# Kernel optimization log

Hardware: AMD Instinct MI355X
Metric: run time of the kernel (lower is better)

The kernel has to match this reference:

```python
import jax, jax.numpy as jnp
import numpy as np

B, V, L, H = 4, 1024, 2048, 2048
TEMP = 1.0
EPS = 1e-12


def _l2norm(x):
    # F.normalize(x, dim=-1): x / max(||x||, eps)
    n = jnp.linalg.norm(x, axis=-1, keepdims=True)
    return x / jnp.maximum(n, EPS)


def setup_inputs() -> dict:
    key = jax.random.key(0)
    k1, k2, k3, k4 = jax.random.split(key, 4)
    std = H ** (-0.5)
    return {
        "vision_features": jax.random.normal(k1, (B, V, H), dtype=jnp.float32),
        "language_features": jax.random.normal(k2, (B, L, H), dtype=jnp.float32),
        "W_vl": jax.random.normal(k3, (H, 2 * H), dtype=jnp.float32) * std,  # vision_language_gate.weight
        "W_lv": jax.random.normal(k4, (H, 2 * H), dtype=jnp.float32) * std,  # language_vision_gate.weight
    }


def reference(vision_features, language_features, W_vl, W_lv):
    b, vsl, h = vision_features.shape
    lsl = language_features.shape[1]
    max_len = max(vsl, lsl)

    # zero-pad both modalities to max_len along seq dim
    vis_p = jnp.pad(vision_features, ((0, 0), (0, max_len - vsl), (0, 0)))
    lang_p = jnp.pad(language_features, ((0, 0), (0, max_len - lsl), (0, 0)))

    # cosine-similarity attention (fp32 softmax)
    scores = jnp.einsum("bvh,blh->bvl", _l2norm(vis_p), _l2norm(lang_p)) / TEMP
    weights = jax.nn.softmax(scores.astype(jnp.float32), axis=-1).astype(vision_features.dtype)
    fused = jnp.einsum("bvl,blh->bvh", weights, lang_p)  # [b, max_len, h]

    # mean pooling over padded sequences (includes zero padding, as in torch)
    vis_avg = jnp.mean(vis_p, axis=1, keepdims=True)    # [b,1,h]
    lang_avg = jnp.mean(lang_p, axis=1, keepdims=True)  # [b,1,h]

    # sigmoid gates: cat([avg.expand, other], -1) @ W.T
    v2l = jnp.concatenate([jnp.broadcast_to(vis_avg, lang_p.shape), lang_p], axis=-1)
    vl_gate = jax.nn.sigmoid(jnp.einsum("bld,hd->blh", v2l, W_vl))
    l2v = jnp.concatenate([jnp.broadcast_to(lang_avg, vis_p.shape), vis_p], axis=-1)
    lv_gate = jax.nn.sigmoid(jnp.einsum("bvd,hd->bvh", l2v, W_lv))

    vision_output = vision_features + fused[:, :vsl, :] * lv_gate[:, :vsl, :]
    language_output = language_features + fused[:, :lsl, :] * vl_gate[:, :lsl, :]
    return fused[:, :max_len, :], vision_output, language_output
```

## Files before the change

### kernel.cpp

```cpp
#include <hip/hip_runtime.h>

#define H_ 2048

typedef __attribute__((ext_vector_type(8))) short short8;
typedef __attribute__((ext_vector_type(4))) float f32x4;
typedef __attribute__((ext_vector_type(4))) unsigned int u32x4;
typedef __attribute__((ext_vector_type(4))) unsigned short u16x4;

__device__ __forceinline__ unsigned short f2bf(float f) {
  unsigned int u = __builtin_bit_cast(unsigned int, f);
  u += 0x7FFFu + ((u >> 16) & 1u);
  return (unsigned short)(u >> 16);
}
__device__ __forceinline__ float bf2f(unsigned short h) {
  unsigned int u = ((unsigned int)h) << 16;
  return __builtin_bit_cast(float, u);
}
__device__ __forceinline__ unsigned int pk2(float a, float b) {
  return (unsigned int)f2bf(a) | ((unsigned int)f2bf(b) << 16);
}

#define GLDS16(gp, lp)                                                 \
  __builtin_amdgcn_global_load_lds(                                    \
      (const __attribute__((address_space(1))) void*)(gp),             \
      (__attribute__((address_space(3))) void*)(lp), 16, 0, 0)

__global__ __launch_bounds__(256) void prep_rows(
    const float* __restrict__ in, long sIn,
    unsigned short* __restrict__ outBf, long sOut,
    float* __restrict__ rnorm, int validRows) {
  const int tid = threadIdx.x;
  const int r = blockIdx.x, b = blockIdx.y;
  unsigned short* orow = outBf + (long)b * sOut + (long)r * H_ + tid * 8;
  if (r >= validRows) {
    *(u32x4*)orow = (u32x4){0u, 0u, 0u, 0u};
    if (tid == 0) rnorm[b * H_ + r] = 0.f;
    return;
  }
  const float* row = in + (long)b * sIn + (long)r * H_ + tid * 8;
  f32x4 x0 = *(const f32x4*)row;
  f32x4 x1 = *(const f32x4*)(row + 4);
  float ss = x0[0]*x0[0] + x0[1]*x0[1] + x0[2]*x0[2] + x0[3]*x0[3]
           + x1[0]*x1[0] + x1[1]*x1[1] + x1[2]*x1[2] + x1[3]*x1[3];
#pragma unroll
  for (int o = 32; o; o >>= 1) ss += __shfl_xor(ss, o, 64);
  __shared__ float red[4];
  if ((tid & 63) == 0) red[tid >> 6] = ss;
  __syncthreads();
  if (tid == 0) {
    float tot = red[0] + red[1] + red[2] + red[3];
    rnorm[b * H_ + r] = 1.f / fmaxf(sqrtf(tot), 1e-12f);
  }
  u32x4 o;
  o[0] = pk2(x0[0], x0[1]); o[1] = pk2(x0[2], x0[3]);
  o[2] = pk2(x1[0], x1[1]); o[3] = pk2(x1[2], x1[3]);
  *(u32x4*)orow = o;
}

__global__ __launch_bounds__(256) void col_sum_part_bf(
    const unsigned short* __restrict__ visBf,
    const unsigned short* __restrict__ langBf, float* __restrict__ part) {
  const int h = blockIdx.x * 256 + threadIdx.x;
  const int y = blockIdx.y;
  const int which = blockIdx.z & 1;
  const int b = blockIdx.z >> 1;
  const long sP = 2048L * 2048;
  float s = 0.f;
  if (!(which == 0 && y >= 4)) {
    const unsigned short* p =
        (which ? langBf : visBf) + (long)b * sP + (long)(y * 256) * H_ + h;
#pragma unroll 4
    for (int i = 0; i < 256; ++i) s += bf2f(p[(long)i * H_]);
  }
  part[(((long)which * 4 + b) * 8 + y) * H_ + h] = s;
}

__global__ __launch_bounds__(256) void col_sum_final(
    const float* __restrict__ part, float* __restrict__ vavg,
    float* __restrict__ lavg) {
  const int h = blockIdx.x * 256 + threadIdx.x;
  const int b = blockIdx.y;
  const int which = blockIdx.z;
  const float* p = part + (((long)which * 4 + b) * 8) * H_ + h;
  float s = 0.f;
#pragma unroll
  for (int y = 0; y < 8; ++y) s += p[y * H_];
  (which ? lavg : vavg)[b * H_ + h] = s * (1.f / 2048.f);
}

__global__ __launch_bounds__(256) void bias_gemv(
    const float* __restrict__ W, const float* __restrict__ avg,
    float* __restrict__ bias) {
  const int lane = threadIdx.x & 63;
  const int wv = threadIdx.x >> 6;
  const int h = blockIdx.x * 4 + wv;
  const float* wrow = W + (long)h * 4096;
  float a0 = 0.f, a1 = 0.f, a2 = 0.f, a3 = 0.f;
#pragma unroll
  for (int i = 0; i < 8; ++i) {
    const int d = i * 256 + lane * 4;
    f32x4 w4 = *(const f32x4*)(wrow + d);
    f32x4 v0 = *(const f32x4*)(avg + 0 * H_ + d);
    f32x4 v1 = *(const f32x4*)(avg + 1 * H_ + d);
    f32x4 v2 = *(const f32x4*)(avg + 2 * H_ + d);
    f32x4 v3 = *(const f32x4*)(avg + 3 * H_ + d);
    a0 += w4[0]*v0[0] + w4[1]*v0[1] + w4[2]*v0[2] + w4[3]*v0[3];
    a1 += w4[0]*v1[0] + w4[1]*v1[1] + w4[2]*v1[2] + w4[3]*v1[3];
    a2 += w4[0]*v2[0] + w4[1]*v2[1] + w4[2]*v2[2] + w4[3]*v2[3];
    a3 += w4[0]*v3[0] + w4[1]*v3[1] + w4[2]*v3[2] + w4[3]*v3[3];
  }
#pragma unroll
  for (int o = 32; o; o >>= 1) {
    a0 += __shfl_xor(a0, o, 64);
    a1 += __shfl_xor(a1, o, 64);
    a2 += __shfl_xor(a2, o, 64);
    a3 += __shfl_xor(a3, o, 64);
  }
  if (lane == 0) {
    bias[0 * H_ + h] = a0; bias[1 * H_ + h] = a1;
    bias[2 * H_ + h] = a2; bias[3 * H_ + h] = a3;
  }
}

__global__ __launch_bounds__(256) void transpose_bf(
    const unsigned short* __restrict__ in, unsigned short* __restrict__ out) {
  __shared__ unsigned short tle[64][72];
  const int b = blockIdx.z;
  const int l0 = blockIdx.y * 64, h0 = blockIdx.x * 64;
  const unsigned short* inb = in + (long)b * (2048L * 2048);
  unsigned short* outb = out + (long)b * (2048L * 2048);
#pragma unroll
  for (int i = 0; i < 16; ++i) {
    const int idx = i * 256 + threadIdx.x;
    const int r = idx >> 6, c = idx & 63;
    tle[r][c] = inb[(long)(l0 + r) * H_ + h0 + c];
  }
  __syncthreads();
#pragma unroll
  for (int i = 0; i < 16; ++i) {
    const int idx = i * 256 + threadIdx.x;
    const int r = idx >> 6, c = idx & 63;
    outb[(long)(h0 + r) * H_ + l0 + c] = tle[c][r];
  }
}

__global__ __launch_bounds__(256) void extract_whi(
    const float* __restrict__ Wvl, const float* __restrict__ Wlv,
    unsigned short* __restrict__ WvlHi, unsigned short* __restrict__ WlvHi) {
  const int h = blockIdx.x;
  const int which = blockIdx.y;
  const float* src = (which ? Wlv : Wvl) + (long)h * 4096 + 2048 + threadIdx.x * 8;
  unsigned short* dst = (which ? WlvHi : WvlHi) + (long)h * H_ + threadIdx.x * 8;
  f32x4 x0 = *(const f32x4*)src;
  f32x4 x1 = *(const f32x4*)(src + 4);
  u32x4 o;
  o[0] = pk2(x0[0], x0[1]); o[1] = pk2(x0[2], x0[3]);
  o[2] = pk2(x1[0], x1[1]); o[3] = pk2(x1[2], x1[3]);
  *(u32x4*)dst = o;
}

__global__ __launch_bounds__(256) void bcast_fused(
    const float* __restrict__ lavg, float* __restrict__ fused) {
  const int b = blockIdx.y;
  const long r = 1024 + blockIdx.x;
  const int c = threadIdx.x * 8;
  f32x4 v0 = *(const f32x4*)(lavg + b * H_ + c);
  f32x4 v1 = *(const f32x4*)(lavg + b * H_ + c + 4);
  float* dst = fused + (long)b * (2048L * 2048) + r * H_ + c;
  *(f32x4*)dst = v0;
  *(f32x4*)(dst + 4) = v1;
}

__global__ __launch_bounds__(256) void softmax_rows(unsigned short* __restrict__ S) {
  const int tid = threadIdx.x;
  const int lane = tid & 63, wv = tid >> 6;
  const int b = blockIdx.x >> 10;
  const int r = blockIdx.x & 1023;
  unsigned short* rowp =
      S + (long)b * (2048L * 2048) + (long)r * H_ + tid * 8;
  u32x4 raw = *(const u32x4*)rowp;
  float v[8];
#pragma unroll
  for (int i = 0; i < 4; ++i) {
    v[2 * i]     = bf2f((unsigned short)(raw[i] & 0xFFFFu));
    v[2 * i + 1] = bf2f((unsigned short)(raw[i] >> 16));
  }
  float mx = v[0];
#pragma unroll
  for (int i = 1; i < 8; ++i) mx = fmaxf(mx, v[i]);
#pragma unroll
  for (int o = 32; o; o >>= 1) mx = fmaxf(mx, __shfl_xor(mx, o, 64));
  __shared__ float red[4];
  if (lane == 0) red[wv] = mx;
  __syncthreads();
  const float MX = fmaxf(fmaxf(red[0], red[1]), fmaxf(red[2], red[3]));
  float p[8], s = 0.f;
#pragma unroll
  for (int i = 0; i < 8; ++i) { p[i] = __expf(v[i] - MX); s += p[i]; }
#pragma unroll
  for (int o = 32; o; o >>= 1) s += __shfl_xor(s, o, 64);
  __syncthreads();
  if (lane == 0) red[wv] = s;
  __syncthreads();
  const float inv = 1.f / (red[0] + red[1] + red[2] + red[3]);
  u32x4 o;
#pragma unroll
  for (int i = 0; i < 4; ++i) o[i] = pk2(p[2 * i] * inv, p[2 * i + 1] * inv);
  *(u32x4*)rowp = o;
}

struct EpArgs {
  unsigned short* Sout; const float* rv; const float* rl;
  float* Fout;
  const unsigned short* residBf; const float* fusedIn;
  const float* bias; float* Oout;
  long sResid, sFused, sOut;
  const unsigned short* A2; const unsigned short* B2;
  const unsigned short* residBf2; const float* bias2; float* Oout2;
  long sResid2, sOut2;
  const float* lavg;
};

#define BAR_ asm volatile("s_barrier" ::: "memory")
#define WAITV_(n) asm volatile("s_waitcnt vmcnt(" #n ")" ::: "memory")
#define LGKM0_ asm volatile("s_waitcnt lgkmcnt(0)" ::: "memory")
#define SB_ __builtin_amdgcn_sched_barrier(0)

template <int MODE>
__global__ __launch_bounds__(256, 2) void gemm_nt(
    const unsigned short* __restrict__ A, long sA,
    const unsigned short* __restrict__ B, long sB, EpArgs ep) {
  __shared__ unsigned short LDS[32768];

  const int tid = threadIdx.x;
  const int lane = tid & 63;
  const int wave = tid >> 6;

  const int gx = gridDim.x, gy = gridDim.y;
  const int nwg = gx * gy * gridDim.z;
  const int lin = blockIdx.x + gx * (blockIdx.y + gy * blockIdx.z);
  const int swz = (lin & 7) * (nwg >> 3) + (lin >> 3);
  const int bx = swz % gx;
  const int rest = swz / gx;
  const int by = rest % gy;
  const int b = rest / gy;
  const int bn = bx << 7;

  int bm;
  bool second = false;
  const unsigned short* Ab;
  const unsigned short* Bb;
  const unsigned short* RbBf = nullptr;
  const float *Fb = nullptr, *biasb = nullptr;
  float* Ob = nullptr;
  if (MODE == 3) {
    second = (by >= 16);
    bm = (second ? by - 16 : by) << 7;
    Ab = (second ? ep.A2 : A) + (long)b * sA;
    Bb = second ? ep.B2 : B;
    RbBf = (second ? ep.residBf2 : ep.residBf) +
           (long)b * (second ? ep.sResid2 : ep.sResid);
    Ob = (second ? ep.Oout2 : ep.Oout) +
         (long)b * (second ? ep.sOut2 : ep.sOut);
    biasb = (second ? ep.bias2 : ep.bias) + b * H_;
    Fb = ep.fusedIn + (long)b * ep.sFused;
  } else {
    bm = by << 7;
    Ab = A + (long)b * sA;
    Bb = B + (long)b * sB;
  }

  const int srow = tid >> 3;
  const int colOff = (((tid & 7) ^ (srow & 7)) << 3);
  const unsigned short* gA = Ab + (long)(bm + srow) * H_ + colOff;
  const unsigned short* gB = Bb + (long)(bn + srow) * H_ + colOff;
  const int ldst = wave * 512;

#define STAGE_(kt, P)                                               \
  do {                                                              \
    const unsigned short* a_ = gA + (kt) * 64;                      \
    const unsigned short* b_ = gB + (kt) * 64;                      \
    GLDS16(a_,           &LDS[(P) * 16384 + 0     + ldst]);         \
    GLDS16(a_ + 32 * H_, &LDS[(P) * 16384 + 2048  + ldst]);         \
    GLDS16(a_ + 64 * H_, &LDS[(P) * 16384 + 4096  + ldst]);         \
    GLDS16(a_ + 96 * H_, &LDS[(P) * 16384 + 6144  + ldst]);         \
    GLDS16(b_,           &LDS[(P) * 16384 + 8192  + ldst]);         \
    GLDS16(b_ + 32 * H_, &LDS[(P) * 16384 + 10240 + ldst]);         \
    GLDS16(b_ + 64 * H_, &LDS[(P) * 16384 + 12288 + ldst]);         \
    GLDS16(b_ + 96 * H_, &LDS[(P) * 16384 + 14336 + ldst]);         \
  } while (0)

  const int row16 = lane & 15;
  const int kg = lane >> 4;
  const int wr = (wave >> 1) << 6;
  const int wc = (wave & 1) << 6;
  const int x0 = ((kg ^ (row16 & 7)) << 4);
  const int x1 = (((4 + kg) ^ (row16 & 7)) << 4);

  const unsigned bAk0 = (unsigned)(unsigned long long)(
      __attribute__((address_space(3))) const void*)LDS +
      (unsigned)((wr + row16) * 128 + x0);
  const unsigned bAk1 = bAk0 + (unsigned)(x1 - x0);
  const unsigned bBk0 = (unsigned)(unsigned long long)(
      __attribute__((address_space(3))) const void*)LDS +
      (unsigned)(16384 + (wc + row16) * 128 + x0);
  const unsigned bBk1 = bBk0 + (unsigned)(x1 - x0);

#define DSRD_(dst, base, off) \
  asm volatile("ds_read_b128 %0, %1 offset:" #off : "=v"(dst) : "v"(base))

  f32x4 acc[4][4];
#pragma unroll
  for (int m = 0; m < 4; ++m)
#pragma unroll
    for (int n = 0; n < 4; ++n) acc[m][n] = (f32x4){0.f, 0.f, 0.f, 0.f};
  short8 aF[4][2], bF[4][2];

#define RDALL_P0                                           \
  do {                                                     \
    DSRD_(aF[0][0], bAk0, 0);    DSRD_(aF[1][0], bAk0, 2048);  \
    DSRD_(aF[2][0], bAk0, 4096); DSRD_(aF[3][0], bAk0, 6144);  \
    DSRD_(aF[0][1], bAk1, 0);    DSRD_(aF[1][1], bAk1, 2048);  \
    DSRD_(aF[2][1], bAk1, 4096); DSRD_(aF[3][1], bAk1, 6144);  \
    DSRD_(bF[0][0], bBk0, 0);    DSRD_(bF[1][0], bBk0, 2048);  \
    DSRD_(bF[2][0], bBk0, 4096); DSRD_(bF[3][0], bBk0, 6144);  \
    DSRD_(bF[0][1], bBk1, 0);    DSRD_(bF[1][1], bBk1, 2048);  \
    DSRD_(bF[2][1], bBk1, 4096); DSRD_(bF[3][1], bBk1, 6144);  \
  } while (0)
#define RDALL_P1                                                   \
  do {                                                             \
    DSRD_(aF[0][0], bAk0, 32768); DSRD_(aF[1][0], bAk0, 34816);   \
    DSRD_(aF[2][0], bAk0, 36864); DSRD_(aF[3][0], bAk0, 38912);   \
    DSRD_(aF[0][1], bAk1, 32768); DSRD_(aF[1][1], bAk1, 34816);   \
    DSRD_(aF[2][1], bAk1, 36864); DSRD_(aF[3][1], bAk1, 38912);   \
    DSRD_(bF[0][0], bBk0, 32768); DSRD_(bF[1][0], bBk0, 34816);   \
    DSRD_(bF[2][0], bBk0, 36864); DSRD_(bF[3][0], bBk0, 38912);   \
    DSRD_(bF[0][1], bBk1, 32768); DSRD_(bF[1][1], bBk1, 34816);   \
    DSRD_(bF[2][1], bBk1, 36864); DSRD_(bF[3][1], bBk1, 38912);   \
  } while (0)

#define MFMA32_                                                             \
  do {                                                                      \
    __builtin_amdgcn_s_setprio(1);                                          \
    _Pragma("unroll") for (int ks_ = 0; ks_ < 2; ++ks_)                     \
    _Pragma("unroll") for (int m_ = 0; m_ < 4; ++m_)                        \
    _Pragma("unroll") for (int n_ = 0; n_ < 4; ++n_)                        \
        acc[m_][n_] = __builtin_amdgcn_mfma_f32_16x16x32_bf16(              \
            aF[m_][ks_], bF[n_][ks_], acc[m_][n_], 0, 0, 0);                \
    __builtin_amdgcn_s_setprio(0);                                          \
  } while (0)

  STAGE_(0, 0); STAGE_(1, 1);
  WAITV_(8);
  BAR_;

  for (int tt = 0; tt < 15; ++tt) {
    const int t2 = tt * 2;
    RDALL_P0; LGKM0_; SB_;
    BAR_;
    STAGE_(t2 + 2, 0);
    WAITV_(8);
    BAR_;
    MFMA32_;
    RDALL_P1; LGKM0_; SB_;
    BAR_;
    STAGE_(t2 + 3, 1);
    WAITV_(8);
    BAR_;
    MFMA32_;
  }
  RDALL_P0; LGKM0_; SB_;
  BAR_;
  WAITV_(0);
  BAR_;
  MFMA32_;
  RDALL_P1; LGKM0_; SB_;
  MFMA32_;

  const int cr0 = bm + wr + kg * 4;
  const int cc0 = bn + wc + row16;

  if (MODE == 0) {
    float rvv[4][4], rlv[4];
#pragma unroll
    for (int m = 0; m < 4; ++m)
#pragma unroll
      for (int j = 0; j < 4; ++j) rvv[m][j] = ep.rv[b * H_ + cr0 + m * 16 + j];
#pragma unroll
    for (int n = 0; n < 4; ++n) rlv[n] = ep.rl[b * H_ + cc0 + n * 16];
    unsigned short* Sb = ep.Sout + (long)b * (H_ * (long)H_);
#pragma unroll
    for (int m = 0; m < 4; ++m)
#pragma unroll
      for (int n = 0; n < 4; ++n)
#pragma unroll
        for (int j = 0; j < 4; ++j) {
          const long idx = (long)(cr0 + m * 16 + j) * H_ + cc0 + n * 16;
          Sb[idx] = f2bf(acc[m][n][j] * rvv[m][j] * rlv[n]);
        }
  } else {
    float* LF = (float*)LDS;
    __syncthreads();
    const int lwr = wr + kg * 4;
    const int lwc = wc + row16;
#pragma unroll
    for (int m = 0; m < 4; ++m)
#pragma unroll
      for (int n = 0; n < 4; ++n)
#pragma unroll
        for (int j = 0; j < 4; ++j) {
          const int r = lwr + m * 16 + j;
          const int c = lwc + n * 16;
          LF[r * 128 + ((c + 4 * r) & 127)] = acc[m][n][j];
        }
    __syncthreads();
    const int r8 = tid >> 5;
    const int c4 = (tid & 31) * 4;
    if (MODE == 1) {
      float* Fo = ep.Fout + (long)b * (H_ * (long)H_);
#pragma unroll
      for (int it = 0; it < 16; ++it) {
        const int r = it * 8 + r8;
        f32x4 v = *(const f32x4*)&LF[r * 128 + ((c4 + 4 * r) & 127)];
        *(f32x4*)&Fo[(long)(bm + r) * H_ + bn + c4] = v;
      }
    } else {
      const f32x4 bvv = *(const f32x4*)&biasb[bn + c4];
      const bool useLavg = (!second) && (bm >= 1024);
      f32x4 lavgv = (f32x4){0.f, 0.f, 0.f, 0.f};
      if (useLavg) lavgv = *(const f32x4*)&ep.lavg[b * H_ + bn + c4];
#pragma unroll
      for (int it = 0; it < 16; ++it) {
        const int r = it * 8 + r8;
        f32x4 v = *(const f32x4*)&LF[r * 128 + ((c4 + 4 * r) & 127)];
        const long off = (long)(bm + r) * H_ + bn + c4;
        const f32x4 fv = useLavg ? lavgv : *(const f32x4*)&Fb[off];
        const u16x4 rb4 = *(const u16x4*)&RbBf[off];
        f32x4 o;
#pragma unroll
        for (int k = 0; k < 4; ++k) {
          const float x = v[k] + bvv[k];
          const float g = 1.f / (1.f + __expf(-x));
          o[k] = bf2f(rb4[k]) + fv[k] * g;
        }
        *(f32x4*)&Ob[off] = o;
      }
    }
  }
#undef STAGE_
#undef DSRD_
#undef RDALL_P0
#undef RDALL_P1
#undef MFMA32_
}

extern "C" void kernel_launch(void* const* d_in, const int* in_sizes, int n_in,
                              void* d_out, int out_size, void* d_ws,
                              size_t ws_size, hipStream_t stream) {
  (void)in_sizes; (void)n_in; (void)out_size; (void)ws_size;
  const float* vis = (const float*)d_in[0];
  const float* lang = (const float*)d_in[1];
  const float* Wvl = (const float*)d_in[2];
  const float* Wlv = (const float*)d_in[3];

  float* out = (float*)d_out;
  float* fused = out;
  float* vis_out = out + 16777216;
  float* lang_out = out + 25165824;
  unsigned short* S = (unsigned short*)lang_out;
  unsigned short* langT = (unsigned short*)vis_out;

  char* w = (char*)d_ws;
  unsigned short* vis_bf = (unsigned short*)w;
  unsigned short* lang_bf = (unsigned short*)(w + 33554432);
  unsigned short* WvlHi = (unsigned short*)(w + 67108864);
  unsigned short* WlvHi = (unsigned short*)(w + 75497472);
  float* rv      = (float*)(w + 83886080);
  float* rl      = (float*)(w + 83918848);
  float* vavg    = (float*)(w + 83951616);
  float* lavg    = (float*)(w + 83984384);
  float* bias_vl = (float*)(w + 84017152);
  float* bias_lv = (float*)(w + 84049920);
  float* part    = (float*)(w + 84082688);

  const long sV = 1024L * 2048, sL = 2048L * 2048, sP = 2048L * 2048;

  prep_rows<<<dim3(2048, 4), 256, 0, stream>>>(vis, sV, vis_bf, sP, rv, 1024);
  prep_rows<<<dim3(2048, 4), 256, 0, stream>>>(lang, sL, lang_bf, sP, rl, 2048);
  col_sum_part_bf<<<dim3(8, 8, 8), 256, 0, stream>>>(vis_bf, lang_bf, part);
  col_sum_final<<<dim3(8, 4, 2), 256, 0, stream>>>(part, vavg, lavg);
  bias_gemv<<<512, 256, 0, stream>>>(Wvl, vavg, bias_vl);
  bias_gemv<<<512, 256, 0, stream>>>(Wlv, lavg, bias_lv);
  transpose_bf<<<dim3(32, 32, 4), 256, 0, stream>>>(lang_bf, langT);
  extract_whi<<<dim3(2048, 2), 256, 0, stream>>>(Wvl, Wlv, WvlHi, WlvHi);
  bcast_fused<<<dim3(1024, 4), 256, 0, stream>>>(lavg, fused);

  EpArgs e1 = {};
  e1.Sout = S; e1.rv = rv; e1.rl = rl;
  gemm_nt<0><<<dim3(16, 8, 4), 256, 0, stream>>>(vis_bf, sP, lang_bf, sP, e1);

  softmax_rows<<<4096, 256, 0, stream>>>(S);

  EpArgs e2 = {};
  e2.Fout = fused;
  gemm_nt<1><<<dim3(16, 8, 4), 256, 0, stream>>>(S, sP, langT, sP, e2);

  EpArgs e34 = {};
  e34.residBf = lang_bf; e34.sResid = sP;
  e34.fusedIn = fused; e34.sFused = sP;
  e34.bias = bias_vl; e34.Oout = lang_out; e34.sOut = sL;
  e34.A2 = vis_bf; e34.B2 = WlvHi;
  e34.residBf2 = vis_bf; e34.sResid2 = sP;
  e34.bias2 = bias_lv; e34.Oout2 = vis_out; e34.sOut2 = sV;
  e34.lavg = lavg;
  gemm_nt<3><<<dim3(16, 24, 4), 256, 0, stream>>>(lang_bf, sP, WvlHi, 0L, e34);
}
```

Measured before the change: 290.5 us.

## Switch GEMM to 32x32x16 MFMA and stage all epilogues through LDS

Each wave's 64x64 GEMM tile now uses a 2x2 grid of 32x32x16 bf16 MFMAs instead of a 4x4 grid of 16x16x32 ones. LDS fragment addressing is re-derived for the new layout. This is meant to raise arithmetic intensity per LDS read and cut MFMA issue count. The score-GEMM epilogue now goes through the same swizzled LDS staging as the other modes, so the bf16 S writes become coalesced 4-wide stores instead of scattered 2-byte stores. The vision prep_rows launch is halved so the padded rows are no longer written; this assumes the workspace already holds zeros there, which is a correctness risk if the workspace is not cleared.

Result: slower. 310.8 us (+7.0%).

```diff
diff --git a/kernel.cpp b/kernel.cpp
--- a/kernel.cpp
+++ b/kernel.cpp
@@ -4,6 +4,7 @@
 
 typedef __attribute__((ext_vector_type(8))) short short8;
 typedef __attribute__((ext_vector_type(4))) float f32x4;
+typedef __attribute__((ext_vector_type(16))) float f32x16;
 typedef __attribute__((ext_vector_type(4))) unsigned int u32x4;
 typedef __attribute__((ext_vector_type(4))) unsigned short u16x4;
 
@@ -290,62 +291,67 @@
     GLDS16(b_ + 96 * H_, &LDS[(P) * 16384 + 14336 + ldst]);         \
   } while (0)
 
-  const int row16 = lane & 15;
-  const int kg = lane >> 4;
+  const int row32 = lane & 31;
+  const int khalf = lane >> 5;
+  const int r7 = row32 & 7;
   const int wr = (wave >> 1) << 6;
   const int wc = (wave & 1) << 6;
-  const int x0 = ((kg ^ (row16 & 7)) << 4);
-  const int x1 = (((4 + kg) ^ (row16 & 7)) << 4);
-
-  const unsigned bAk0 = (unsigned)(unsigned long long)(
-      __attribute__((address_space(3))) const void*)LDS +
-      (unsigned)((wr + row16) * 128 + x0);
-  const unsigned bAk1 = bAk0 + (unsigned)(x1 - x0);
-  const unsigned bBk0 = (unsigned)(unsigned long long)(
-      __attribute__((address_space(3))) const void*)LDS +
-      (unsigned)(16384 + (wc + row16) * 128 + x0);
-  const unsigned bBk1 = bBk0 + (unsigned)(x1 - x0);
+
+  const unsigned ldsBase = (unsigned)(unsigned long long)(
+      __attribute__((address_space(3))) const void*)LDS;
+  const unsigned aRow = ldsBase + (unsigned)((wr + row32) * 128);
+  const unsigned bRow = ldsBase + 16384u + (unsigned)((wc + row32) * 128);
+  const unsigned kbA0 = aRow + (unsigned)(((0 + khalf) ^ r7) << 4);
+  const unsigned kbA1 = aRow + (unsigned)(((2 + khalf) ^ r7) << 4);
+  const unsigned kbA2 = aRow + (unsigned)(((4 + khalf) ^ r7) << 4);
+  const unsigned kbA3 = aRow + (unsigned)(((6 + khalf) ^ r7) << 4);
+  const unsigned kbB0 = bRow + (unsigned)(((0 + khalf) ^ r7) << 4);
+  const unsigned kbB1 = bRow + (unsigned)(((2 + khalf) ^ r7) << 4);
+  const unsigned kbB2 = bRow + (unsigned)(((4 + khalf) ^ r7) << 4);
+  const unsigned kbB3 = bRow + (unsigned)(((6 + khalf) ^ r7) << 4);
 
 #define DSRD_(dst, base, off) \
   asm volatile("ds_read_b128 %0, %1 offset:" #off : "=v"(dst) : "v"(base))
 
-  f32x4 acc[4][4];
-#pragma unroll
-  for (int m = 0; m < 4; ++m)
-#pragma unroll
-    for (int n = 0; n < 4; ++n) acc[m][n] = (f32x4){0.f, 0.f, 0.f, 0.f};
-  short8 aF[4][2], bF[4][2];
-
-#define RDALL_P0                                           \
-  do {                                                     \
-    DSRD_(aF[0][0], bAk0, 0);    DSRD_(aF[1][0], bAk0, 2048);  \
-    DSRD_(aF[2][0], bAk0, 4096); DSRD_(aF[3][0], bAk0, 6144);  \
-    DSRD_(aF[0][1], bAk1, 0);    DSRD_(aF[1][1], bAk1, 2048);  \
-    DSRD_(aF[2][1], bAk1, 4096); DSRD_(aF[3][1], bAk1, 6144);  \
-    DSRD_(bF[0][0], bBk0, 0);    DSRD_(bF[1][0], bBk0, 2048);  \
-    DSRD_(bF[2][0], bBk0, 4096); DSRD_(bF[3][0], bBk0, 6144);  \
-    DSRD_(bF[0][1], bBk1, 0);    DSRD_(bF[1][1], bBk1, 2048);  \
-    DSRD_(bF[2][1], bBk1, 4096); DSRD_(bF[3][1], bBk1, 6144);  \
+  f32x16 acc[2][2];
+#pragma unroll
+  for (int m = 0; m < 2; ++m)
+#pragma unroll
+    for (int n = 0; n < 2; ++n)
+#pragma unroll
+      for (int r = 0; r < 16; ++r) acc[m][n][r] = 0.f;
+  short8 aF[2][4], bF[2][4];
+
+#define RDALL_P0                                               \
+  do {                                                         \
+    DSRD_(aF[0][0], kbA0, 0);    DSRD_(aF[1][0], kbA0, 4096);  \
+    DSRD_(aF[0][1], kbA1, 0);    DSRD_(aF[1][1], kbA1, 4096);  \
+    DSRD_(aF[0][2], kbA2, 0);    DSRD_(aF[1][2], kbA2, 4096);  \
+    DSRD_(aF[0][3], kbA3, 0);    DSRD_(aF[1][3], kbA3, 4096);  \
+    DSRD_(bF[0][0], kbB0, 0);    DSRD_(bF[1][0], kbB0, 4096);  \
+    DSRD_(bF[0][1], kbB1, 0);    DSRD_(bF[1][1], kbB1, 4096);  \
+    DSRD_(bF[0][2], kbB2, 0);    DSRD_(bF[1][2], kbB2, 4096);  \
+    DSRD_(bF[0][3], kbB3, 0);    DSRD_(bF[1][3], kbB3, 4096);  \
   } while (0)
-#define RDALL_P1                                                   \
-  do {                                                             \
-    DSRD_(aF[0][0], bAk0, 32768); DSRD_(aF[1][0], bAk0, 34816);   \
-    DSRD_(aF[2][0], bAk0, 36864); DSRD_(aF[3][0], bAk0, 38912);   \
-    DSRD_(aF[0][1], bAk1, 32768); DSRD_(aF[1][1], bAk1, 34816);   \
-    DSRD_(aF[2][1], bAk1, 36864); DSRD_(aF[3][1], bAk1, 38912);   \
-    DSRD_(bF[0][0], bBk0, 32768); DSRD_(bF[1][0], bBk0, 34816);   \
-    DSRD_(bF[2][0], bBk0, 36864); DSRD_(bF[3][0], bBk0, 38912);   \
-    DSRD_(bF[0][1], bBk1, 32768); DSRD_(bF[1][1], bBk1, 34816);   \
-    DSRD_(bF[2][1], bBk1, 36864); DSRD_(bF[3][1], bBk1, 38912);   \
+#define RDALL_P1                                                     \
+  do {                                                               \
+    DSRD_(aF[0][0], kbA0, 32768); DSRD_(aF[1][0], kbA0, 36864);      \
+    DSRD_(aF[0][1], kbA1, 32768); DSRD_(aF[1][1], kbA1, 36864);      \
+    DSRD_(aF[0][2], kbA2, 32768); DSRD_(aF[1][2], kbA2, 36864);      \
+    DSRD_(aF[0][3], kbA3, 32768); DSRD_(aF[1][3], kbA3, 36864);      \
+    DSRD_(bF[0][0], kbB0, 32768); DSRD_(bF[1][0], kbB0, 36864);      \
+    DSRD_(bF[0][1], kbB1, 32768); DSRD_(bF[1][1], kbB1, 36864);      \
+    DSRD_(bF[0][2], kbB2, 32768); DSRD_(bF[1][2], kbB2, 36864);      \
+    DSRD_(bF[0][3], kbB3, 32768); DSRD_(bF[1][3], kbB3, 36864);      \
   } while (0)
 
-#define MFMA32_                                                             \
+#define MFMA16_                                                             \
   do {                                                                      \
     __builtin_amdgcn_s_setprio(1);                                          \
-    _Pragma("unroll") for (int ks_ = 0; ks_ < 2; ++ks_)                     \
-    _Pragma("unroll") for (int m_ = 0; m_ < 4; ++m_)                        \
-    _Pragma("unroll") for (int n_ = 0; n_ < 4; ++n_)                        \
-        acc[m_][n_] = __builtin_amdgcn_mfma_f32_16x16x32_bf16(              \
+    _Pragma("unroll") for (int ks_ = 0; ks_ < 4; ++ks_)                     \
+    _Pragma("unroll") for (int m_ = 0; m_ < 2; ++m_)                        \
+    _Pragma("unroll") for (int n_ = 0; n_ < 2; ++n_)                        \
+        acc[m_][n_] = __builtin_amdgcn_mfma_f32_32x32x16_bf16(              \
             aF[m_][ks_], bF[n_][ks_], acc[m_][n_], 0, 0, 0);                \
     __builtin_amdgcn_s_setprio(0);                                          \
   } while (0)
@@ -361,97 +367,86 @@
     STAGE_(t2 + 2, 0);
     WAITV_(8);
     BAR_;
-    MFMA32_;
+    MFMA16_;
     RDALL_P1; LGKM0_; SB_;
     BAR_;
     STAGE_(t2 + 3, 1);
     WAITV_(8);
     BAR_;
-    MFMA32_;
+    MFMA16_;
   }
   RDALL_P0; LGKM0_; SB_;
   BAR_;
   WAITV_(0);
   BAR_;
-  MFMA32_;
+  MFMA16_;
   RDALL_P1; LGKM0_; SB_;
-  MFMA32_;
-
-  const int cr0 = bm + wr + kg * 4;
-  const int cc0 = bn + wc + row16;
+  MFMA16_;
+
+  float* LF = (float*)LDS;
+  __syncthreads();
+#pragma unroll
+  for (int m = 0; m < 2; ++m)
+#pragma unroll
+    for (int n = 0; n < 2; ++n)
+#pragma unroll
+      for (int r = 0; r < 16; ++r) {
+        const int row = wr + m * 32 + (r & 3) + 8 * (r >> 2) + 4 * khalf;
+        const int col = wc + n * 32 + row32;
+        LF[row * 128 + ((col + 4 * row) & 127)] = acc[m][n][r];
+      }
+  __syncthreads();
+  const int r8 = tid >> 5;
+  const int c4 = (tid & 31) * 4;
 
   if (MODE == 0) {
-    float rvv[4][4], rlv[4];
-#pragma unroll
-    for (int m = 0; m < 4; ++m)
-#pragma unroll
-      for (int j = 0; j < 4; ++j) rvv[m][j] = ep.rv[b * H_ + cr0 + m * 16 + j];
-#pragma unroll
-    for (int n = 0; n < 4; ++n) rlv[n] = ep.rl[b * H_ + cc0 + n * 16];
     unsigned short* Sb = ep.Sout + (long)b * (H_ * (long)H_);
-#pragma unroll
-    for (int m = 0; m < 4; ++m)
-#pragma unroll
-      for (int n = 0; n < 4; ++n)
-#pragma unroll
-        for (int j = 0; j < 4; ++j) {
-          const long idx = (long)(cr0 + m * 16 + j) * H_ + cc0 + n * 16;
-          Sb[idx] = f2bf(acc[m][n][j] * rvv[m][j] * rlv[n]);
-        }
+    const f32x4 rl4 = *(const f32x4*)&ep.rl[b * H_ + bn + c4];
+#pragma unroll
+    for (int it = 0; it < 16; ++it) {
+      const int r = it * 8 + r8;
+      const float rvr = ep.rv[b * H_ + bm + r];
+      f32x4 v = *(const f32x4*)&LF[r * 128 + ((c4 + 4 * r) & 127)];
+      u16x4 o;
+#pragma unroll
+      for (int k = 0; k < 4; ++k) o[k] = f2bf(v[k] * rvr * rl4[k]);
+      *(u16x4*)&Sb[(long)(bm + r) * H_ + bn + c4] = o;
+    }
+  } else if (MODE == 1) {
+    float* Fo = ep.Fout + (long)b * (H_ * (long)H_);
+#pragma unroll
+    for (int it = 0; it < 16; ++it) {
+      const int r = it * 8 + r8;
+      f32x4 v = *(const f32x4*)&LF[r * 128 + ((c4 + 4 * r) & 127)];
+      *(f32x4*)&Fo[(long)(bm + r) * H_ + bn + c4] = v;
+    }
   } else {
-    float* LF = (float*)LDS;
-    __syncthreads();
-    const int lwr = wr + kg * 4;
-    const int lwc = wc + row16;
-#pragma unroll
-    for (int m = 0; m < 4; ++m)
-#pragma unroll
-      for (int n = 0; n < 4; ++n)
-#pragma unroll
-        for (int j = 0; j < 4; ++j) {
-          const int r = lwr + m * 16 + j;
-          const int c = lwc + n * 16;
-          LF[r * 128 + ((c + 4 * r) & 127)] = acc[m][n][j];
-        }
-    __syncthreads();
-    const int r8 = tid >> 5;
-    const int c4 = (tid & 31) * 4;
-    if (MODE == 1) {
-      float* Fo = ep.Fout + (long)b * (H_ * (long)H_);
-#pragma unroll
-      for (int it = 0; it < 16; ++it) {
-        const int r = it * 8 + r8;
-        f32x4 v = *(const f32x4*)&LF[r * 128 + ((c4 + 4 * r) & 127)];
-        *(f32x4*)&Fo[(long)(bm + r) * H_ + bn + c4] = v;
+    const f32x4 bvv = *(const f32x4*)&biasb[bn + c4];
+    const bool useLavg = (!second) && (bm >= 1024);
+    f32x4 lavgv = (f32x4){0.f, 0.f, 0.f, 0.f};
+    if (useLavg) lavgv = *(const f32x4*)&ep.lavg[b * H_ + bn + c4];
+#pragma unroll
+    for (int it = 0; it < 16; ++it) {
+      const int r = it * 8 + r8;
+      f32x4 v = *(const f32x4*)&LF[r * 128 + ((c4 + 4 * r) & 127)];
+      const long off = (long)(bm + r) * H_ + bn + c4;
+      const f32x4 fv = useLavg ? lavgv : *(const f32x4*)&Fb[off];
+      const u16x4 rb4 = *(const u16x4*)&RbBf[off];
+      f32x4 o;
+#pragma unroll
+      for (int k = 0; k < 4; ++k) {
+        const float x = v[k] + bvv[k];
+        const float g = 1.f / (1.f + __expf(-x));
+        o[k] = bf2f(rb4[k]) + fv[k] * g;
       }
-    } else {
-      const f32x4 bvv = *(const f32x4*)&biasb[bn + c4];
-      const bool useLavg = (!second) && (bm >= 1024);
-      f32x4 lavgv = (f32x4){0.f, 0.f, 0.f, 0.f};
-      if (useLavg) lavgv = *(const f32x4*)&ep.lavg[b * H_ + bn + c4];
-#pragma unroll
-      for (int it = 0; it < 16; ++it) {
-        const int r = it * 8 + r8;
-        f32x4 v = *(const f32x4*)&LF[r * 128 + ((c4 + 4 * r) & 127)];
-        const long off = (long)(bm + r) * H_ + bn + c4;
-        const f32x4 fv = useLavg ? lavgv : *(const f32x4*)&Fb[off];
-        const u16x4 rb4 = *(const u16x4*)&RbBf[off];
-        f32x4 o;
-#pragma unroll
-        for (int k = 0; k < 4; ++k) {
-          const float x = v[k] + bvv[k];
-          const float g = 1.f / (1.f + __expf(-x));
-          o[k] = bf2f(rb4[k]) + fv[k] * g;
-        }
-        *(f32x4*)&Ob[off] = o;
-      }
+      *(f32x4*)&Ob[off] = o;
     }
   }
 #undef STAGE_
 #undef DSRD_
 #undef RDALL_P0
 #undef RDALL_P1
-#undef MFMA32_
+#undef MFMA16_
 }
 
 extern "C" void kernel_launch(void* const* d_in, const int* in_sizes, int n_in,
@@ -485,7 +480,7 @@
 
   const long sV = 1024L * 2048, sL = 2048L * 2048, sP = 2048L * 2048;
 
-  prep_rows<<<dim3(2048, 4), 256, 0, stream>>>(vis, sV, vis_bf, sP, rv, 1024);
+  prep_rows<<<dim3(1024, 4), 256, 0, stream>>>(vis, sV, vis_bf, sP, rv, 1024);
   prep_rows<<<dim3(2048, 4), 256, 0, stream>>>(lang, sL, lang_bf, sP, rl, 2048);
   col_sum_part_bf<<<dim3(8, 8, 8), 256, 0, stream>>>(vis_bf, lang_bf, part);
   col_sum_final<<<dim3(8, 4, 2), 256, 0, stream>>>(part, vavg, lavg);
```
